# Optimization experiments

Measured on AMD Instinct MI355X. Metric: run time of the kernel, lower is better.

Reference implementation:

```python
import jax, jax.numpy as jnp
import numpy as np

N_HEADS = 16
D_HEAD = 64
D_MODEL = 1024
WINDOW = 256
B, T = 4, 2048


def rotate_half(x):
    x1, x2 = jnp.split(x, 2, axis=-1)
    return jnp.concatenate([-x2, x1], axis=-1)


def apply_rope(x, cos, sin):
    return x * cos + rotate_half(x) * sin


def setup_inputs() -> dict:
    key = jax.random.key(0)
    ks = jax.random.split(key, 5)
    x = jax.random.normal(ks[0], (B, T, D_MODEL), dtype=jnp.float32)
    cos = jax.random.normal(ks[1], (1, T, 1, D_HEAD), dtype=jnp.float32)
    sin = jax.random.normal(ks[2], (1, T, 1, D_HEAD), dtype=jnp.float32)
    qkv_w = jax.random.normal(ks[3], (3 * D_MODEL, D_MODEL), dtype=jnp.float32) * (D_MODEL ** -0.5)
    out_w = jax.random.normal(ks[4], (D_MODEL, D_MODEL), dtype=jnp.float32) * (D_MODEL ** -0.5)
    return {"x": x, "cos": cos, "sin": sin, "qkv_w": qkv_w, "out_w": out_w}


def reference(x, cos, sin, qkv_w, out_w):
    Bc, Tc, C = x.shape
    # QKV projection (bias-free Linear: y = x @ W^T)
    qkv = jnp.einsum('btc,fc->btf', x, qkv_w)
    q, k, v = jnp.split(qkv, 3, axis=-1)
    # [B, H, T, d]
    def to_heads(t):
        return t.reshape(Bc, Tc, N_HEADS, D_HEAD).transpose(0, 2, 1, 3)
    q, k, v = to_heads(q), to_heads(k), to_heads(v)
    # RoPE: cos/sin [1, T, 1, d] -> [1, 1, T, d] broadcasting over heads
    cos_t = cos[:, :Tc].transpose(0, 2, 1, 3)
    sin_t = sin[:, :Tc].transpose(0, 2, 1, 3)
    q = apply_rope(q, cos_t, sin_t)
    k = apply_rope(k, cos_t, sin_t)
    # banded causal mask: allow j <= i and j >= i - (window-1)
    i = jnp.arange(Tc)[:, None]
    j = jnp.arange(Tc)[None, :]
    allowed = (j <= i) & (j >= i - (WINDOW - 1))  # [T, T]
    scale = 1.0 / jnp.sqrt(jnp.asarray(D_HEAD, dtype=q.dtype))
    scores = jnp.einsum('bhqd,bhkd->bhqk', q, k) * scale
    scores = jnp.where(allowed[None, None], scores, jnp.finfo(scores.dtype).min)
    attn = jax.nn.softmax(scores, axis=-1)
    out = jnp.einsum('bhqk,bhkd->bhqd', attn, v)
    out = out.transpose(0, 2, 1, 3).reshape(Bc, Tc, C)
    return jnp.einsum('btc,oc->bto', out, out_w)
```

## Files before the change

kernel.cpp:

```cpp
#include <hip/hip_runtime.h>

typedef __bf16 bf16_t;
typedef __bf16 bf16x8 __attribute__((ext_vector_type(8)));
typedef __bf16 bf16x4 __attribute__((ext_vector_type(4)));
typedef float f32x4 __attribute__((ext_vector_type(4)));

#define GLOAD_LDS16(gptr, lptr)                                                              \
  __builtin_amdgcn_global_load_lds((const __attribute__((address_space(1))) void*)(gptr),    \
                                   (__attribute__((address_space(3))) void*)(lptr), 16, 0, 0)

__device__ __forceinline__ f32x4 f32x4_zero() {
  f32x4 v; v[0] = 0.f; v[1] = 0.f; v[2] = 0.f; v[3] = 0.f; return v;
}

__device__ __forceinline__ int kxr(int r) { return (r & 7) ^ (((r >> 3) & 3) << 1); }

__device__ __forceinline__ void rope8(const bf16x8 xl, const bf16x8 xh,
                                      const float* __restrict__ cosb,
                                      const float* __restrict__ sinb, float sc,
                                      bf16x8& ol, bf16x8& oh) {
  float4 cl0 = *(const float4*)(cosb);
  float4 cl1 = *(const float4*)(cosb + 4);
  float4 ch0 = *(const float4*)(cosb + 32);
  float4 ch1 = *(const float4*)(cosb + 36);
  float4 sl0 = *(const float4*)(sinb);
  float4 sl1 = *(const float4*)(sinb + 4);
  float4 sh0 = *(const float4*)(sinb + 32);
  float4 sh1 = *(const float4*)(sinb + 36);
  float cl[8] = {cl0.x, cl0.y, cl0.z, cl0.w, cl1.x, cl1.y, cl1.z, cl1.w};
  float ch[8] = {ch0.x, ch0.y, ch0.z, ch0.w, ch1.x, ch1.y, ch1.z, ch1.w};
  float sl[8] = {sl0.x, sl0.y, sl0.z, sl0.w, sl1.x, sl1.y, sl1.z, sl1.w};
  float sh[8] = {sh0.x, sh0.y, sh0.z, sh0.w, sh1.x, sh1.y, sh1.z, sh1.w};
#pragma unroll
  for (int e = 0; e < 8; e++) {
    float a = (float)xl[e], b = (float)xh[e];
    ol[e] = (bf16_t)((a * cl[e] - b * sl[e]) * sc);
    oh[e] = (bf16_t)((b * ch[e] + a * sh[e]) * sc);
  }
}

__global__ void cast3_kernel(const float* __restrict__ a, const float* __restrict__ b,
                             const float* __restrict__ c, bf16_t* __restrict__ oa,
                             bf16_t* __restrict__ ob, bf16_t* __restrict__ oc) {
  int i = blockIdx.x * blockDim.x + threadIdx.x;
  const float* src; bf16_t* dst; int j;
  if (i < 2097152) { src = a; dst = oa; j = i; }
  else if (i < 2883584) { src = b; dst = ob; j = i - 2097152; }
  else { src = c; dst = oc; j = i - 2883584; }
  float4 v = ((const float4*)src)[j];
  bf16x4 o;
  o[0] = (bf16_t)v.x; o[1] = (bf16_t)v.y; o[2] = (bf16_t)v.z; o[3] = (bf16_t)v.w;
  ((bf16x4*)dst)[j] = o;
}

__global__ __launch_bounds__(256) void rope_k_kernel(bf16_t* __restrict__ kh,
                                                     const float* __restrict__ cosp,
                                                     const float* __restrict__ sinp) {
  int idx = blockIdx.x * 256 + threadIdx.x;
  int qo = idx & 3;
  int row = idx >> 2;
  int t = row & 2047;
  bf16x8* base = (bf16x8*)(kh + (size_t)row * 64);
  bf16x8 lo = base[qo], hi = base[qo + 4];
  bf16x8 ol, oh;
  rope8(lo, hi, cosp + t * 64 + qo * 8, sinp + t * 64 + qo * 8, 1.0f, ol, oh);
  base[qo] = ol;
  base[qo + 4] = oh;
}

#define GT_AELE 16384
#define GT_BELE 8192
#define GT_TILE (GT_AELE + GT_BELE)

__device__ __forceinline__ void gt_stage(const bf16_t* __restrict__ A,
                                         const bf16_t* __restrict__ B, bf16_t* buf,
                                         int bm, int bn, int t, int K, int tid) {
#pragma unroll
  for (int i = 0; i < 4; i++) {
    int gi = tid + i * 512;
    int row = gi >> 3, g = gi & 7;
    const bf16_t* src = A + (size_t)(bm * 256 + row) * K + t * 64 + ((g ^ (row & 7)) << 3);
    GLOAD_LDS16(src, buf + gi * 8);
  }
#pragma unroll
  for (int i = 0; i < 2; i++) {
    int gi = tid + i * 512;
    int row = gi >> 3, g = gi & 7;
    const bf16_t* src = B + (size_t)(bn * 128 + row) * K + t * 64 + ((g ^ (row & 7)) << 3);
    GLOAD_LDS16(src, buf + GT_AELE + gi * 8);
  }
}

template <int MODE>
__global__ __launch_bounds__(512, 1) void gemm_bt_kernel(
    const bf16_t* __restrict__ A, const bf16_t* __restrict__ B, float* __restrict__ C,
    bf16_t* __restrict__ oq, bf16_t* __restrict__ ok_, bf16_t* __restrict__ ov,
    int M, int N, int K) {
  __shared__ bf16_t lds[3 * GT_TILE];

  const int tid = threadIdx.x;
  const int lane = tid & 63;
  const int wid = tid >> 6;
  const int wr = wid >> 1;
  const int wc = wid & 1;
  const int l16 = lane & 15;
  const int qd = lane >> 4;
  const int bm = blockIdx.x, bn = blockIdx.y;

  f32x4 acc[4][4];
#pragma unroll
  for (int m = 0; m < 4; m++)
#pragma unroll
    for (int n = 0; n < 4; n++) acc[m][n] = f32x4_zero();

  const int NT = K >> 6;

  gt_stage(A, B, lds, bm, bn, 0, K, tid);
  gt_stage(A, B, lds + GT_TILE, bm, bn, 1, K, tid);
  asm volatile("s_waitcnt vmcnt(6)" ::: "memory");
  __builtin_amdgcn_s_barrier();
  __builtin_amdgcn_sched_barrier(0);

  int s = 0;
  for (int j = 0; j < NT; ++j) {
    if (j + 2 < NT) {
      int s2 = s + 2; if (s2 >= 3) s2 -= 3;
      gt_stage(A, B, lds + s2 * GT_TILE, bm, bn, j + 2, K, tid);
    }

    const bf16_t* bufc = lds + s * GT_TILE;
    bf16x8 af[4][2], bf[4][2];
#pragma unroll
    for (int m = 0; m < 4; m++)
#pragma unroll
      for (int kk = 0; kk < 2; kk++) {
        int row = wr * 64 + m * 16 + l16;
        af[m][kk] = *(const bf16x8*)&bufc[row * 64 + (((kk * 4 + qd) ^ (row & 7)) << 3)];
      }
#pragma unroll
    for (int n = 0; n < 4; n++)
#pragma unroll
      for (int kk = 0; kk < 2; kk++) {
        int row = wc * 64 + n * 16 + l16;
        bf[n][kk] = *(const bf16x8*)&bufc[GT_AELE + row * 64 + (((kk * 4 + qd) ^ (row & 7)) << 3)];
      }

    __builtin_amdgcn_s_setprio(1);
#pragma unroll
    for (int m = 0; m < 4; m++)
#pragma unroll
      for (int n = 0; n < 4; n++)
#pragma unroll
        for (int kk = 0; kk < 2; kk++)
          acc[m][n] = __builtin_amdgcn_mfma_f32_16x16x32_bf16(af[m][kk], bf[n][kk], acc[m][n], 0, 0, 0);
    __builtin_amdgcn_s_setprio(0);

    if (j + 2 < NT) {
      asm volatile("s_waitcnt vmcnt(6)" ::: "memory");
    } else {
      asm volatile("s_waitcnt vmcnt(0)" ::: "memory");
    }
    __builtin_amdgcn_s_barrier();
    __builtin_amdgcn_sched_barrier(0);
    s = (s == 2) ? 0 : s + 1;
  }

  if (MODE == 0) {
#pragma unroll
    for (int m = 0; m < 4; m++)
#pragma unroll
      for (int n = 0; n < 4; n++)
#pragma unroll
        for (int r = 0; r < 4; r++) {
          int row = bm * 256 + wr * 64 + m * 16 + qd * 4 + r;
          int col = bn * 128 + wc * 64 + n * 16 + l16;
          C[(size_t)row * N + col] = acc[m][n][r];
        }
  } else {
    const int colbase = bn * 128 + wc * 64;
    const int part = colbase >> 10;
    const int h = (colbase & 1023) >> 6;
    bf16_t* dst = (part == 0) ? oq : (part == 1) ? ok_ : ov;
#pragma unroll
    for (int m = 0; m < 4; m++)
#pragma unroll
      for (int r = 0; r < 4; r++) {
        int row = bm * 256 + wr * 64 + m * 16 + qd * 4 + r;
        int b = row >> 11, t = row & 2047;
        size_t basei = (((size_t)(b * 16 + h)) * 2048 + t) * 64;
#pragma unroll
        for (int n = 0; n < 4; n++)
          dst[basei + n * 16 + l16] = (bf16_t)acc[m][n][r];
      }
  }
}

__global__ __launch_bounds__(256) void attn_kernel(
    const bf16_t* __restrict__ qh, const bf16_t* __restrict__ kh,
    const bf16_t* __restrict__ vh, bf16_t* __restrict__ ao,
    const float* __restrict__ cosp, const float* __restrict__ sinp) {
  __shared__ bf16_t qs[64 * 64];
  __shared__ bf16_t ks[64 * 64];
  __shared__ bf16_t vs[64 * 64];
  __shared__ bf16_t vswz[8 * 64 * 8];
  __shared__ bf16_t ps[4][16 * 64];

  const int tid = threadIdx.x;
  const int lane = tid & 63;
  const int wid = tid >> 6;
  const int l16 = lane & 15;
  const int qd = lane >> 4;

  const int bh = blockIdx.x;
  const int i0 = blockIdx.y * 64;
  const int b = bh >> 4, h = bh & 15;

  auto swz4 = [](int f) { int r = f >> 3; return r * 8 + ((f & 7) ^ (r & 7)); };
  const int r0 = tid >> 3, q0 = tid & 7;
  const int rr = tid >> 2, qo = tid & 3;

  {
    const bf16x8* src = (const bf16x8*)(qh + ((size_t)bh * 2048 + i0) * 64);
    bf16x8* dst = (bf16x8*)qs;
    const int fl = rr * 8 + qo, fh = fl + 4;
    bf16x8 ol, oh;
    rope8(src[fl], src[fh], cosp + (i0 + rr) * 64 + qo * 8, sinp + (i0 + rr) * 64 + qo * 8,
          0.18033688011112042f, ol, oh);
    dst[swz4(fl)] = ol;
    dst[swz4(fh)] = oh;
  }

  bf16x8 bones;
#pragma unroll
  for (int e = 0; e < 8; e++) bones[e] = (bf16_t)1.0f;

  float l_i[4] = {0.f, 0.f, 0.f, 0.f};
  f32x4 oacc[4];
#pragma unroll
  for (int nb = 0; nb < 4; nb++) oacc[nb] = f32x4_zero();

  const int c1 = i0 >> 6;
  const int c0 = (c1 >= 4) ? (c1 - 4) : 0;
  const size_t bhbase = (size_t)bh * 2048;

  uint4 kr0, kr1, vr0, vr1;
  {
    const uint4* ksrc = (const uint4*)(kh + (bhbase + (size_t)c0 * 64) * 64);
    const uint4* vsrc = (const uint4*)(vh + (bhbase + (size_t)c0 * 64) * 64);
    kr0 = ksrc[tid]; kr1 = ksrc[tid + 256];
    vr0 = vsrc[tid]; vr1 = vsrc[tid + 256];
  }

  for (int c = c0; c <= c1; c++) {
    const int j0 = c * 64;
    __syncthreads();
    {
      uint4* kdst = (uint4*)ks;
      uint4* vdst = (uint4*)vs;
      kdst[swz4(tid)] = kr0;
      kdst[swz4(tid + 256)] = kr1;
      vdst[r0 * 8 + (q0 ^ kxr(r0))] = vr0;
      vdst[(r0 + 32) * 8 + (q0 ^ kxr(r0 + 32))] = vr1;
    }
    if (c < c1) {
      const uint4* ksrc = (const uint4*)(kh + (bhbase + (size_t)(c + 1) * 64) * 64);
      const uint4* vsrc = (const uint4*)(vh + (bhbase + (size_t)(c + 1) * 64) * 64);
      kr0 = ksrc[tid]; kr1 = ksrc[tid + 256];
      vr0 = vsrc[tid]; vr1 = vsrc[tid + 256];
    }
    __syncthreads();

    f32x4 sacc[4];
#pragma unroll
    for (int nb = 0; nb < 4; nb++) sacc[nb] = f32x4_zero();
#pragma unroll
    for (int kk = 0; kk < 2; kk++) {
      bf16x8 afr = *(const bf16x8*)&qs[(wid * 16 + l16) * 64 + (((kk * 4 + qd) ^ (l16 & 7)) * 8)];
#pragma unroll
      for (int nb = 0; nb < 4; nb++) {
        bf16x8 bfr = *(const bf16x8*)&ks[(nb * 16 + l16) * 64 + (((kk * 4 + qd) ^ (l16 & 7)) * 8)];
        sacc[nb] = __builtin_amdgcn_mfma_f32_16x16x32_bf16(afr, bfr, sacc[nb], 0, 0, 0);
      }
    }

#pragma unroll
    for (int p2 = 0; p2 < 2; p2++) {
      int combo = p2 * 4 + wid;
      int jbase = (combo >> 2) * 32 + (lane >> 4) * 8;
      int dcol = (combo & 3) * 16 + (lane & 15);
      int bb = dcol >> 3, dlo = dcol & 7;
      bf16x8 v8;
#pragma unroll
      for (int e = 0; e < 8; e++) {
        int row = jbase + e;
        v8[e] = vs[row * 64 + ((bb ^ kxr(row)) * 8) + dlo];
      }
      *(bf16x8*)&vswz[(combo * 64 + lane) * 8] = v8;
    }

#pragma unroll
    for (int r = 0; r < 4; r++) {
      const int i = i0 + wid * 16 + qd * 4 + r;
      const int prow = qd * 4 + r;
#pragma unroll
      for (int nb = 0; nb < 4; nb++) {
        const int j = j0 + nb * 16 + l16;
        bool valid = (j <= i) && (j + 256 > i);
        float p = valid ? exp2f(sacc[nb][r]) : 0.f;
        ps[wid][prow * 64 + (((nb * 2 + (l16 >> 3)) ^ (prow & 7)) * 8) + (l16 & 7)] = (bf16_t)p;
      }
    }

    __syncthreads();

    f32x4 lacc = f32x4_zero();
#pragma unroll
    for (int kk = 0; kk < 2; kk++) {
      bf16x8 afr = *(const bf16x8*)&ps[wid][l16 * 64 + (((kk * 4 + qd) ^ (l16 & 7)) * 8)];
      lacc = __builtin_amdgcn_mfma_f32_16x16x32_bf16(afr, bones, lacc, 0, 0, 0);
#pragma unroll
      for (int nb = 0; nb < 4; nb++) {
        bf16x8 bfr = *(const bf16x8*)&vswz[((kk * 4 + nb) * 64 + lane) * 8];
        oacc[nb] = __builtin_amdgcn_mfma_f32_16x16x32_bf16(afr, bfr, oacc[nb], 0, 0, 0);
      }
    }
#pragma unroll
    for (int r = 0; r < 4; r++) l_i[r] += lacc[r];
  }

#pragma unroll
  for (int nb = 0; nb < 4; nb++) {
#pragma unroll
    for (int r = 0; r < 4; r++) {
      int t = i0 + wid * 16 + qd * 4 + r;
      ao[((size_t)(b * 2048 + t)) * 1024 + h * 64 + nb * 16 + l16] =
          (bf16_t)(oacc[nb][r] / l_i[r]);
    }
  }
}

extern "C" void kernel_launch(void* const* d_in, const int* in_sizes, int n_in,
                              void* d_out, int out_size, void* d_ws, size_t ws_size,
                              hipStream_t stream) {
  const float* x    = (const float*)d_in[0];
  const float* cosp = (const float*)d_in[1];
  const float* sinp = (const float*)d_in[2];
  const float* qkvw = (const float*)d_in[3];
  const float* outw = (const float*)d_in[4];
  float* out = (float*)d_out;

  char* ws = (char*)d_ws;
  bf16_t* xb  = (bf16_t*)(ws + 0);
  bf16_t* qwb = (bf16_t*)(ws + 16777216);
  bf16_t* owb = (bf16_t*)(ws + 23068672);
  bf16_t* qhp = (bf16_t*)(ws + 25165824);
  bf16_t* khp = (bf16_t*)(ws + 41943040);
  bf16_t* vhp = (bf16_t*)(ws + 58720256);
  bf16_t* aop = (bf16_t*)(ws + 75497472);

  cast3_kernel<<<12288, 256, 0, stream>>>(x, qkvw, outw, xb, qwb, owb);

  gemm_bt_kernel<1><<<dim3(32, 24), 512, 0, stream>>>(xb, qwb, nullptr, qhp, khp, vhp,
                                                      8192, 3072, 1024);
  rope_k_kernel<<<2048, 256, 0, stream>>>(khp, cosp, sinp);
  attn_kernel<<<dim3(64, 32), 256, 0, stream>>>(qhp, khp, vhp, aop, cosp, sinp);
  gemm_bt_kernel<0><<<dim3(32, 8), 512, 0, stream>>>(aop, owb, out, nullptr, nullptr, nullptr,
                                                     8192, 1024, 1024);
}
```

Baseline: 224.0 us.

## Interleave GEMM prefetch chunks with MFMA sub-phases in the main loop

Splits each K-step of the bf16 GEMM into four phases. Each phase loads a slice of A/B fragments from LDS, issues a quarter of the next-next tile's global-to-LDS loads, then runs a smaller MFMA batch. The goal is to spread global loads and LDS reads across the compute so memory and matrix-core work overlap more evenly. In exchange it adds more barriers per K-step (two per phase), which could add synchronisation overhead.

```diff
diff --git a/kernel.cpp b/kernel.cpp
--- a/kernel.cpp
+++ b/kernel.cpp
@@ -72,23 +72,31 @@
 #define GT_BELE 8192
 #define GT_TILE (GT_AELE + GT_BELE)
 
+__device__ __forceinline__ void gt_stage_chunk(const bf16_t* __restrict__ A,
+                                               const bf16_t* __restrict__ B, bf16_t* buf,
+                                               int bm, int bn, int t, int K, int tid,
+                                               int phase) {
+  if (phase < 2) {
+#pragma unroll
+    for (int i = 0; i < 2; i++) {
+      int gi = tid + (phase * 2 + i) * 512;
+      int row = gi >> 3, g = gi & 7;
+      const bf16_t* src = A + (size_t)(bm * 256 + row) * K + t * 64 + ((g ^ (row & 7)) << 3);
+      GLOAD_LDS16(src, buf + gi * 8);
+    }
+  } else {
+    int gi = tid + (phase - 2) * 512;
+    int row = gi >> 3, g = gi & 7;
+    const bf16_t* src = B + (size_t)(bn * 128 + row) * K + t * 64 + ((g ^ (row & 7)) << 3);
+    GLOAD_LDS16(src, buf + GT_AELE + gi * 8);
+  }
+}
+
 __device__ __forceinline__ void gt_stage(const bf16_t* __restrict__ A,
                                          const bf16_t* __restrict__ B, bf16_t* buf,
                                          int bm, int bn, int t, int K, int tid) {
 #pragma unroll
-  for (int i = 0; i < 4; i++) {
-    int gi = tid + i * 512;
-    int row = gi >> 3, g = gi & 7;
-    const bf16_t* src = A + (size_t)(bm * 256 + row) * K + t * 64 + ((g ^ (row & 7)) << 3);
-    GLOAD_LDS16(src, buf + gi * 8);
-  }
-#pragma unroll
-  for (int i = 0; i < 2; i++) {
-    int gi = tid + i * 512;
-    int row = gi >> 3, g = gi & 7;
-    const bf16_t* src = B + (size_t)(bn * 128 + row) * K + t * 64 + ((g ^ (row & 7)) << 3);
-    GLOAD_LDS16(src, buf + GT_AELE + gi * 8);
-  }
+  for (int p = 0; p < 4; p++) gt_stage_chunk(A, B, buf, bm, bn, t, K, tid, p);
 }
 
 template <int MODE>
@@ -123,45 +131,55 @@
 
   int s = 0;
   for (int j = 0; j < NT; ++j) {
-    if (j + 2 < NT) {
-      int s2 = s + 2; if (s2 >= 3) s2 -= 3;
-      gt_stage(A, B, lds + s2 * GT_TILE, bm, bn, j + 2, K, tid);
-    }
-
     const bf16_t* bufc = lds + s * GT_TILE;
-    bf16x8 af[4][2], bf[4][2];
-#pragma unroll
-    for (int m = 0; m < 4; m++)
-#pragma unroll
-      for (int kk = 0; kk < 2; kk++) {
-        int row = wr * 64 + m * 16 + l16;
-        af[m][kk] = *(const bf16x8*)&bufc[row * 64 + (((kk * 4 + qd) ^ (row & 7)) << 3)];
-      }
-#pragma unroll
-    for (int n = 0; n < 4; n++)
-#pragma unroll
-      for (int kk = 0; kk < 2; kk++) {
-        int row = wc * 64 + n * 16 + l16;
-        bf[n][kk] = *(const bf16x8*)&bufc[GT_AELE + row * 64 + (((kk * 4 + qd) ^ (row & 7)) << 3)];
-      }
-
-    __builtin_amdgcn_s_setprio(1);
-#pragma unroll
-    for (int m = 0; m < 4; m++)
-#pragma unroll
-      for (int n = 0; n < 4; n++)
-#pragma unroll
-        for (int kk = 0; kk < 2; kk++)
-          acc[m][n] = __builtin_amdgcn_mfma_f32_16x16x32_bf16(af[m][kk], bf[n][kk], acc[m][n], 0, 0, 0);
-    __builtin_amdgcn_s_setprio(0);
-
-    if (j + 2 < NT) {
-      asm volatile("s_waitcnt vmcnt(6)" ::: "memory");
-    } else {
-      asm volatile("s_waitcnt vmcnt(0)" ::: "memory");
-    }
-    __builtin_amdgcn_s_barrier();
-    __builtin_amdgcn_sched_barrier(0);
+    int s2 = s + 2; if (s2 >= 3) s2 -= 3;
+    bf16_t* bufn = lds + s2 * GT_TILE;
+    const bool pre = (j + 2 < NT);
+
+    bf16x8 afr[4], bfr[2];
+#pragma unroll
+    for (int kk = 0; kk < 2; kk++) {
+#pragma unroll
+      for (int nh = 0; nh < 2; nh++) {
+        const int ph = kk * 2 + nh;
+        if (nh == 0) {
+#pragma unroll
+          for (int m = 0; m < 4; m++) {
+            int row = wr * 64 + m * 16 + l16;
+            afr[m] = *(const bf16x8*)&bufc[row * 64 + (((kk * 4 + qd) ^ (row & 7)) << 3)];
+          }
+        }
+#pragma unroll
+        for (int n = 0; n < 2; n++) {
+          int row = wc * 64 + (nh * 2 + n) * 16 + l16;
+          bfr[n] = *(const bf16x8*)&bufc[GT_AELE + row * 64 + (((kk * 4 + qd) ^ (row & 7)) << 3)];
+        }
+        if (pre) gt_stage_chunk(A, B, bufn, bm, bn, j + 2, K, tid, ph);
+
+        __builtin_amdgcn_s_barrier();
+        asm volatile("s_waitcnt lgkmcnt(0)" ::: "memory");
+        __builtin_amdgcn_sched_barrier(0);
+
+        __builtin_amdgcn_s_setprio(1);
+#pragma unroll
+        for (int m = 0; m < 4; m++)
+#pragma unroll
+          for (int n = 0; n < 2; n++)
+            acc[m][nh * 2 + n] =
+                __builtin_amdgcn_mfma_f32_16x16x32_bf16(afr[m], bfr[n], acc[m][nh * 2 + n], 0, 0, 0);
+        __builtin_amdgcn_s_setprio(0);
+
+        if (ph == 3) {
+          if (pre) {
+            asm volatile("s_waitcnt vmcnt(6)" ::: "memory");
+          } else {
+            asm volatile("s_waitcnt vmcnt(0)" ::: "memory");
+          }
+        }
+        __builtin_amdgcn_s_barrier();
+        __builtin_amdgcn_sched_barrier(0);
+      }
+    }
     s = (s == 2) ? 0 : s + 1;
   }
 
```

New measurement: 223.1 us. Within noise of the previous version (-0.4%).

## Fuse RoPE into QKV GEMM epilogue and drop separate K rope pass

Applied to the files above, without the earlier changes.

Applies RoPE (and the softmax scale for Q) directly in the QKV projection GEMM epilogue, removing the standalone rope_k kernel and the rope work in the attention prologue. Attention now copies Q straight into shared memory. The K/V register prefetch of the next chunk is also removed in favour of loading each chunk directly inside the loop. This saves a kernel launch and a read-modify-write pass over K, at the cost of scalar cos/sin loads in the epilogue and less latency hiding in attention.

```diff
diff --git a/kernel.cpp b/kernel.cpp
--- a/kernel.cpp
+++ b/kernel.cpp
@@ -14,30 +14,6 @@
 }
 
 __device__ __forceinline__ int kxr(int r) { return (r & 7) ^ (((r >> 3) & 3) << 1); }
-
-__device__ __forceinline__ void rope8(const bf16x8 xl, const bf16x8 xh,
-                                      const float* __restrict__ cosb,
-                                      const float* __restrict__ sinb, float sc,
-                                      bf16x8& ol, bf16x8& oh) {
-  float4 cl0 = *(const float4*)(cosb);
-  float4 cl1 = *(const float4*)(cosb + 4);
-  float4 ch0 = *(const float4*)(cosb + 32);
-  float4 ch1 = *(const float4*)(cosb + 36);
-  float4 sl0 = *(const float4*)(sinb);
-  float4 sl1 = *(const float4*)(sinb + 4);
-  float4 sh0 = *(const float4*)(sinb + 32);
-  float4 sh1 = *(const float4*)(sinb + 36);
-  float cl[8] = {cl0.x, cl0.y, cl0.z, cl0.w, cl1.x, cl1.y, cl1.z, cl1.w};
-  float ch[8] = {ch0.x, ch0.y, ch0.z, ch0.w, ch1.x, ch1.y, ch1.z, ch1.w};
-  float sl[8] = {sl0.x, sl0.y, sl0.z, sl0.w, sl1.x, sl1.y, sl1.z, sl1.w};
-  float sh[8] = {sh0.x, sh0.y, sh0.z, sh0.w, sh1.x, sh1.y, sh1.z, sh1.w};
-#pragma unroll
-  for (int e = 0; e < 8; e++) {
-    float a = (float)xl[e], b = (float)xh[e];
-    ol[e] = (bf16_t)((a * cl[e] - b * sl[e]) * sc);
-    oh[e] = (bf16_t)((b * ch[e] + a * sh[e]) * sc);
-  }
-}
 
 __global__ void cast3_kernel(const float* __restrict__ a, const float* __restrict__ b,
                              const float* __restrict__ c, bf16_t* __restrict__ oa,
@@ -53,21 +29,6 @@
   ((bf16x4*)dst)[j] = o;
 }
 
-__global__ __launch_bounds__(256) void rope_k_kernel(bf16_t* __restrict__ kh,
-                                                     const float* __restrict__ cosp,
-                                                     const float* __restrict__ sinp) {
-  int idx = blockIdx.x * 256 + threadIdx.x;
-  int qo = idx & 3;
-  int row = idx >> 2;
-  int t = row & 2047;
-  bf16x8* base = (bf16x8*)(kh + (size_t)row * 64);
-  bf16x8 lo = base[qo], hi = base[qo + 4];
-  bf16x8 ol, oh;
-  rope8(lo, hi, cosp + t * 64 + qo * 8, sinp + t * 64 + qo * 8, 1.0f, ol, oh);
-  base[qo] = ol;
-  base[qo + 4] = oh;
-}
-
 #define GT_AELE 16384
 #define GT_BELE 8192
 #define GT_TILE (GT_AELE + GT_BELE)
@@ -95,6 +56,7 @@
 __global__ __launch_bounds__(512, 1) void gemm_bt_kernel(
     const bf16_t* __restrict__ A, const bf16_t* __restrict__ B, float* __restrict__ C,
     bf16_t* __restrict__ oq, bf16_t* __restrict__ ok_, bf16_t* __restrict__ ov,
+    const float* __restrict__ cosp, const float* __restrict__ sinp,
     int M, int N, int K) {
   __shared__ bf16_t lds[3 * GT_TILE];
 
@@ -181,24 +143,45 @@
     const int part = colbase >> 10;
     const int h = (colbase & 1023) >> 6;
     bf16_t* dst = (part == 0) ? oq : (part == 1) ? ok_ : ov;
-#pragma unroll
-    for (int m = 0; m < 4; m++)
-#pragma unroll
-      for (int r = 0; r < 4; r++) {
-        int row = bm * 256 + wr * 64 + m * 16 + qd * 4 + r;
-        int b = row >> 11, t = row & 2047;
-        size_t basei = (((size_t)(b * 16 + h)) * 2048 + t) * 64;
-#pragma unroll
-        for (int n = 0; n < 4; n++)
-          dst[basei + n * 16 + l16] = (bf16_t)acc[m][n][r];
-      }
+    if (part == 2) {
+#pragma unroll
+      for (int m = 0; m < 4; m++)
+#pragma unroll
+        for (int r = 0; r < 4; r++) {
+          int row = bm * 256 + wr * 64 + m * 16 + qd * 4 + r;
+          int b = row >> 11, t = row & 2047;
+          size_t basei = (((size_t)(b * 16 + h)) * 2048 + t) * 64;
+#pragma unroll
+          for (int n = 0; n < 4; n++)
+            dst[basei + n * 16 + l16] = (bf16_t)acc[m][n][r];
+        }
+    } else {
+      const float qsc = (part == 0) ? 0.18033688011112042f : 1.0f;
+#pragma unroll
+      for (int m = 0; m < 4; m++)
+#pragma unroll
+        for (int r = 0; r < 4; r++) {
+          int row = bm * 256 + wr * 64 + m * 16 + qd * 4 + r;
+          int b = row >> 11, t = row & 2047;
+          size_t basei = (((size_t)(b * 16 + h)) * 2048 + t) * 64;
+#pragma unroll
+          for (int nb = 0; nb < 2; nb++) {
+            int d = nb * 16 + l16;
+            float xl = acc[m][nb][r];
+            float xh = acc[m][nb + 2][r];
+            float cl = cosp[t * 64 + d], ch = cosp[t * 64 + d + 32];
+            float sl = sinp[t * 64 + d], sh = sinp[t * 64 + d + 32];
+            dst[basei + d]      = (bf16_t)((xl * cl - xh * sl) * qsc);
+            dst[basei + d + 32] = (bf16_t)((xh * ch + xl * sh) * qsc);
+          }
+        }
+    }
   }
 }
 
 __global__ __launch_bounds__(256) void attn_kernel(
     const bf16_t* __restrict__ qh, const bf16_t* __restrict__ kh,
-    const bf16_t* __restrict__ vh, bf16_t* __restrict__ ao,
-    const float* __restrict__ cosp, const float* __restrict__ sinp) {
+    const bf16_t* __restrict__ vh, bf16_t* __restrict__ ao) {
   __shared__ bf16_t qs[64 * 64];
   __shared__ bf16_t ks[64 * 64];
   __shared__ bf16_t vs[64 * 64];
@@ -217,17 +200,12 @@
 
   auto swz4 = [](int f) { int r = f >> 3; return r * 8 + ((f & 7) ^ (r & 7)); };
   const int r0 = tid >> 3, q0 = tid & 7;
-  const int rr = tid >> 2, qo = tid & 3;
 
   {
-    const bf16x8* src = (const bf16x8*)(qh + ((size_t)bh * 2048 + i0) * 64);
-    bf16x8* dst = (bf16x8*)qs;
-    const int fl = rr * 8 + qo, fh = fl + 4;
-    bf16x8 ol, oh;
-    rope8(src[fl], src[fh], cosp + (i0 + rr) * 64 + qo * 8, sinp + (i0 + rr) * 64 + qo * 8,
-          0.18033688011112042f, ol, oh);
-    dst[swz4(fl)] = ol;
-    dst[swz4(fh)] = oh;
+    const uint4* src = (const uint4*)(qh + ((size_t)bh * 2048 + i0) * 64);
+    uint4* dst = (uint4*)qs;
+    dst[swz4(tid)] = src[tid];
+    dst[swz4(tid + 256)] = src[tid + 256];
   }
 
   bf16x8 bones;
@@ -241,32 +219,17 @@
 
   const int c1 = i0 >> 6;
   const int c0 = (c1 >= 4) ? (c1 - 4) : 0;
-  const size_t bhbase = (size_t)bh * 2048;
-
-  uint4 kr0, kr1, vr0, vr1;
-  {
-    const uint4* ksrc = (const uint4*)(kh + (bhbase + (size_t)c0 * 64) * 64);
-    const uint4* vsrc = (const uint4*)(vh + (bhbase + (size_t)c0 * 64) * 64);
-    kr0 = ksrc[tid]; kr1 = ksrc[tid + 256];
-    vr0 = vsrc[tid]; vr1 = vsrc[tid + 256];
-  }
 
   for (int c = c0; c <= c1; c++) {
     const int j0 = c * 64;
     __syncthreads();
     {
-      uint4* kdst = (uint4*)ks;
-      uint4* vdst = (uint4*)vs;
-      kdst[swz4(tid)] = kr0;
-      kdst[swz4(tid + 256)] = kr1;
-      vdst[r0 * 8 + (q0 ^ kxr(r0))] = vr0;
-      vdst[(r0 + 32) * 8 + (q0 ^ kxr(r0 + 32))] = vr1;
-    }
-    if (c < c1) {
-      const uint4* ksrc = (const uint4*)(kh + (bhbase + (size_t)(c + 1) * 64) * 64);
-      const uint4* vsrc = (const uint4*)(vh + (bhbase + (size_t)(c + 1) * 64) * 64);
-      kr0 = ksrc[tid]; kr1 = ksrc[tid + 256];
-      vr0 = vsrc[tid]; vr1 = vsrc[tid + 256];
+      const uint4* ksrc = (const uint4*)(kh + ((size_t)bh * 2048 + j0) * 64);
+      const uint4* vsrc = (const uint4*)(vh + ((size_t)bh * 2048 + j0) * 64);
+      uint4* kdst = (uint4*)ks; uint4* vdst = (uint4*)vs;
+      kdst[swz4(tid)] = ksrc[tid]; kdst[swz4(tid + 256)] = ksrc[tid + 256];
+      vdst[r0 * 8 + (q0 ^ kxr(r0))] = vsrc[tid];
+      vdst[(r0 + 32) * 8 + (q0 ^ kxr(r0 + 32))] = vsrc[tid + 256];
     }
     __syncthreads();
 
@@ -361,9 +324,8 @@
   cast3_kernel<<<12288, 256, 0, stream>>>(x, qkvw, outw, xb, qwb, owb);
 
   gemm_bt_kernel<1><<<dim3(32, 24), 512, 0, stream>>>(xb, qwb, nullptr, qhp, khp, vhp,
-                                                      8192, 3072, 1024);
-  rope_k_kernel<<<2048, 256, 0, stream>>>(khp, cosp, sinp);
-  attn_kernel<<<dim3(64, 32), 256, 0, stream>>>(qhp, khp, vhp, aop, cosp, sinp);
+                                                      cosp, sinp, 8192, 3072, 1024);
+  attn_kernel<<<dim3(64, 32), 256, 0, stream>>>(qhp, khp, vhp, aop);
   gemm_bt_kernel<0><<<dim3(32, 8), 512, 0, stream>>>(aop, owb, out, nullptr, nullptr, nullptr,
-                                                     8192, 1024, 1024);
-}
+                                                     nullptr, nullptr, 8192, 1024, 1024);
+}
```

After: 219.0 us. 1.02x faster.
